# Kernel tuning notes

Hardware: AMD Instinct MI355X
Metric: run time of the kernel (lower is better)

The kernel has to match this reference:

```python
import jax, jax.numpy as jnp
import numpy as np

IN_FEATURES = 4096
OUT_FEATURES = 14336
TOPK_RATIO = 0.3
TOPK = int(IN_FEATURES * TOPK_RATIO)  # 1228


def setup_inputs() -> dict:
    key = jax.random.key(0)
    k1, k2, k3 = jax.random.split(key, 3)
    x = jax.random.normal(k1, (1, 1, IN_FEATURES), dtype=jnp.float32)
    weight = jax.random.normal(k2, (OUT_FEATURES, IN_FEATURES), dtype=jnp.float32)
    bias = jax.random.normal(k3, (OUT_FEATURES,), dtype=jnp.float32)
    return {"x": x, "weight": weight, "bias": bias}


def reference(x, weight, bias):
    # Decode path (bsz*seq == 1), first-call cache miss: indices come from
    # the current activation's top-k |x| values (recall==1.0 branch).
    bsz, seq, _ = x.shape
    xf = x.reshape(-1)  # [in_features]
    # argsort(|x|, descending)[:topk] == top_k on |x| (tie order irrelevant for the math)
    _, idx = jax.lax.top_k(jnp.abs(xf).astype(jnp.float32), TOPK)  # [topk]
    x_slice = xf[idx]                 # [topk]
    w_slice = weight[:, idx]          # [out_features, topk]
    # x[:, indices] @ weight_slice.T + bias
    out = jnp.einsum("k,ok->o", x_slice, w_slice) + bias  # [out_features]
    return out.reshape(bsz, seq, OUT_FEATURES)
```

## Files before the change

### kernel.cpp

```cpp
#include <hip/hip_runtime.h>
#include <hip/hip_bf16.h>

#define N_IN 4096
#define N_OUT 14336
#define TOPK 1228

__global__ __launch_bounds__(1024) void topk_mask_kernel(
    const float* __restrict__ x, float* __restrict__ x_masked) {
  __shared__ unsigned int s_abs[N_IN];
  __shared__ unsigned int s_hist[256];
  __shared__ unsigned int s_scan[256];
  __shared__ unsigned int s_prefix;
  __shared__ unsigned int s_krem;
  __shared__ unsigned long long s_cmask[N_IN / 64];
  __shared__ unsigned int s_cbase[N_IN / 64];

  const int tid = threadIdx.x;
  const int lane = tid & 63;

#pragma unroll
  for (int it = 0; it < N_IN / 1024; ++it) {
    const int i = it * 1024 + tid;
    s_abs[i] = __float_as_uint(x[i]) & 0x7fffffffu;
  }
  if (tid == 0) { s_prefix = 0u; s_krem = TOPK; }
  __syncthreads();

  for (int pass = 3; pass >= 0; --pass) {
    if (tid < 256) s_hist[tid] = 0u;
    __syncthreads();
    const int shift = pass * 8;
    const unsigned int maskAbove =
        (pass == 3) ? 0u : (0xFFFFFFFFu << (shift + 8));
    const unsigned int prefix = s_prefix;
    const unsigned int krem = s_krem;

#pragma unroll
    for (int it = 0; it < N_IN / 1024; ++it) {
      const int i = it * 1024 + tid;
      const unsigned int b = s_abs[i];
      const bool active = ((b & maskAbove) == prefix);
      const unsigned int bucket = (b >> shift) & 0xFFu;
      unsigned long long m = __ballot(active);
#pragma unroll
      for (int bit = 0; bit < 8; ++bit) {
        const unsigned long long vote =
            __ballot(active && ((bucket >> bit) & 1u));
        m &= ((bucket >> bit) & 1u) ? vote : ~vote;
      }
      if (active) {
        const int leader = __ffsll((unsigned long long)m) - 1;
        if (lane == leader)
          atomicAdd(&s_hist[bucket], (unsigned int)__popcll(m));
      }
    }
    __syncthreads();

    if (tid < 256) s_scan[tid] = s_hist[255 - tid];
    __syncthreads();
    for (int off = 1; off < 256; off <<= 1) {
      unsigned int v = 0u;
      if (tid < 256 && tid >= off) v = s_scan[tid - off];
      __syncthreads();
      if (tid < 256) s_scan[tid] += v;
      __syncthreads();
    }
    if (tid < 256) {
      const unsigned int t = (unsigned int)tid;
      const unsigned int C = s_scan[255 - t];
      const unsigned int S = (t == 255u) ? 0u : s_scan[254 - t];
      if (S < krem && C >= krem) {
        s_prefix = prefix | (t << shift);
        s_krem = krem - S;
      }
    }
    __syncthreads();
  }

  const unsigned int t_abs = s_prefix;
  const unsigned int need = s_krem;

#pragma unroll
  for (int it = 0; it < N_IN / 1024; ++it) {
    const int i = it * 1024 + tid;
    const bool eq = (s_abs[i] == t_abs);
    const unsigned long long m = __ballot(eq);
    if (lane == 0) s_cmask[i >> 6] = m;
  }
  __syncthreads();
  if (tid < 64) {
    const unsigned int cnt = (unsigned int)__popcll(s_cmask[tid]);
    unsigned int inc = cnt;
#pragma unroll
    for (int off = 1; off < 64; off <<= 1) {
      const unsigned int v = __shfl_up(inc, off, 64);
      if (lane >= off) inc += v;
    }
    s_cbase[tid] = inc - cnt;
  }
  __syncthreads();

#pragma unroll
  for (int it = 0; it < N_IN / 1024; ++it) {
    const int i = it * 1024 + tid;
    const unsigned int b = s_abs[i];
    bool sel = (b > t_abs);
    if (b == t_abs) {
      const unsigned long long below =
          s_cmask[i >> 6] & ((1ull << lane) - 1ull);
      sel = (s_cbase[i >> 6] + (unsigned int)__popcll(below)) < need;
    }
    x_masked[i] = sel ? x[i] : 0.0f;
  }
}

__global__ __launch_bounds__(256) void masked_matvec_kernel(
    const float* __restrict__ xm, const float* __restrict__ W,
    const float* __restrict__ bias, float* __restrict__ out) {
  __shared__ float s_x[N_IN];

  const int tid = threadIdx.x;
  for (int i = tid; i < N_IN; i += 256) s_x[i] = xm[i];
  __syncthreads();

  const int wave = tid >> 6;
  const int lane = tid & 63;
  const int row = blockIdx.x * 4 + wave;
  const float* wr = W + (size_t)row * N_IN;

  float acc = 0.0f;
#pragma unroll
  for (int it = 0; it < N_IN / 256; ++it) {
    const int base = it * 256 + lane * 4;
    const float4 w = *reinterpret_cast<const float4*>(wr + base);
    const float4 xv = *reinterpret_cast<const float4*>(&s_x[base]);
    acc += w.x * xv.x + w.y * xv.y + w.z * xv.z + w.w * xv.w;
  }

#pragma unroll
  for (int off = 32; off >= 1; off >>= 1) acc += __shfl_down(acc, off, 64);

  if (lane == 0) out[row] = acc + bias[row];
}

extern "C" void kernel_launch(void* const* d_in, const int* in_sizes, int n_in,
                              void* d_out, int out_size, void* d_ws,
                              size_t ws_size, hipStream_t stream) {
  const float* x    = (const float*)d_in[0];
  const float* W    = (const float*)d_in[1];
  const float* bias = (const float*)d_in[2];
  float* out = (float*)d_out;
  float* xm  = (float*)d_ws;

  topk_mask_kernel<<<1, 1024, 0, stream>>>(x, xm);
  masked_matvec_kernel<<<N_OUT / 4, 256, 0, stream>>>(xm, W, bias, out);
}
```

Before: 58.13 us.

## Fuse top-k selection into matvec blocks and prefetch weight rows early

Merges the single-block top-k mask kernel and the matvec kernel into one launch. Each of the 3584 blocks now recomputes the radix select on its own shared copy of x. The first weight loads are issued before the selection so they overlap it. The 256-bin scan is replaced by a wave-level shuffle scan, and a fast path skips tie handling when all threshold-equal elements are needed. This removes the serialized single-block kernel and the extra launch, but every block repeats the selection work, which could lengthen per-block latency on a kernel that is bandwidth-bound.

```diff
diff --git a/kernel.cpp b/kernel.cpp
--- a/kernel.cpp
+++ b/kernel.cpp
@@ -4,43 +4,58 @@
 #define N_IN 4096
 #define N_OUT 14336
 #define TOPK 1228
+#define PF 4
 
-__global__ __launch_bounds__(1024) void topk_mask_kernel(
-    const float* __restrict__ x, float* __restrict__ x_masked) {
-  __shared__ unsigned int s_abs[N_IN];
-  __shared__ unsigned int s_hist[256];
-  __shared__ unsigned int s_scan[256];
-  __shared__ unsigned int s_prefix;
-  __shared__ unsigned int s_krem;
+__global__ __launch_bounds__(256) void fused_topk_matvec_kernel(
+    const float* __restrict__ x, const float* __restrict__ W,
+    const float* __restrict__ bias, float* __restrict__ out) {
+  __shared__ __align__(16) float s_x[N_IN];
+  __shared__ __align__(16) unsigned int s_hist[256];
+  __shared__ unsigned int s_pk[4];
   __shared__ unsigned long long s_cmask[N_IN / 64];
   __shared__ unsigned int s_cbase[N_IN / 64];
 
   const int tid = threadIdx.x;
+  const int wave = tid >> 6;
   const int lane = tid & 63;
+  const int row = blockIdx.x * 4 + wave;
 
-#pragma unroll
-  for (int it = 0; it < N_IN / 1024; ++it) {
-    const int i = it * 1024 + tid;
-    s_abs[i] = __float_as_uint(x[i]) & 0x7fffffffu;
-  }
-  if (tid == 0) { s_prefix = 0u; s_krem = TOPK; }
+  const float4* __restrict__ x4 = reinterpret_cast<const float4*>(x);
+  const float4* __restrict__ wr4 =
+      reinterpret_cast<const float4*>(W + (size_t)row * N_IN);
+  float4* s_x4 = reinterpret_cast<float4*>(s_x);
+
+  float4 xv0 = x4[0 * 256 + tid];
+  float4 xv1 = x4[1 * 256 + tid];
+  float4 xv2 = x4[2 * 256 + tid];
+  float4 xv3 = x4[3 * 256 + tid];
+  float4 w0 = wr4[0 * 64 + lane];
+  float4 w1 = wr4[1 * 64 + lane];
+  float4 w2 = wr4[2 * 64 + lane];
+  float4 w3 = wr4[3 * 64 + lane];
+
+  s_x4[0 * 256 + tid] = xv0;
+  s_x4[1 * 256 + tid] = xv1;
+  s_x4[2 * 256 + tid] = xv2;
+  s_x4[3 * 256 + tid] = xv3;
+  if (tid == 0) { s_pk[0] = 0u; s_pk[1] = TOPK; }
   __syncthreads();
 
   for (int pass = 3; pass >= 0; --pass) {
-    if (tid < 256) s_hist[tid] = 0u;
+    const unsigned int prefix = s_pk[0];
+    const unsigned int krem = s_pk[1];
+    s_hist[tid] = 0u;
     __syncthreads();
+
     const int shift = pass * 8;
     const unsigned int maskAbove =
         (pass == 3) ? 0u : (0xFFFFFFFFu << (shift + 8));
-    const unsigned int prefix = s_prefix;
-    const unsigned int krem = s_krem;
 
-#pragma unroll
-    for (int it = 0; it < N_IN / 1024; ++it) {
-      const int i = it * 1024 + tid;
-      const unsigned int b = s_abs[i];
-      const bool active = ((b & maskAbove) == prefix);
-      const unsigned int bucket = (b >> shift) & 0xFFu;
+    for (int r = 0; r < 16; ++r) {
+      const unsigned int ub =
+          __float_as_uint(s_x[r * 256 + tid]) & 0x7fffffffu;
+      const bool active = ((ub & maskAbove) == prefix);
+      const unsigned int bucket = (ub >> shift) & 0xFFu;
       unsigned long long m = __ballot(active);
 #pragma unroll
       for (int bit = 0; bit < 8; ++bit) {
@@ -56,84 +71,95 @@
     }
     __syncthreads();
 
-    if (tid < 256) s_scan[tid] = s_hist[255 - tid];
-    __syncthreads();
-    for (int off = 1; off < 256; off <<= 1) {
-      unsigned int v = 0u;
-      if (tid < 256 && tid >= off) v = s_scan[tid - off];
-      __syncthreads();
-      if (tid < 256) s_scan[tid] += v;
-      __syncthreads();
-    }
-    if (tid < 256) {
-      const unsigned int t = (unsigned int)tid;
-      const unsigned int C = s_scan[255 - t];
-      const unsigned int S = (t == 255u) ? 0u : s_scan[254 - t];
-      if (S < krem && C >= krem) {
-        s_prefix = prefix | (t << shift);
-        s_krem = krem - S;
+    if (tid < 64) {
+      const unsigned int h0 = s_hist[tid * 4 + 0];
+      const unsigned int h1 = s_hist[tid * 4 + 1];
+      const unsigned int h2 = s_hist[tid * 4 + 2];
+      const unsigned int h3 = s_hist[tid * 4 + 3];
+      const unsigned int s = h0 + h1 + h2 + h3;
+      unsigned int inc = s;
+#pragma unroll
+      for (int off = 1; off < 64; off <<= 1) {
+        const unsigned int v = __shfl_down(inc, off, 64);
+        if (tid + off < 64) inc += v;
+      }
+      const unsigned int U = inc - s;
+      const unsigned int C3 = U + h3;
+      const unsigned int C2 = C3 + h2;
+      const unsigned int C1 = C2 + h1;
+      const unsigned int C0 = C1 + h0;
+      const unsigned int Carr[4] = {C0, C1, C2, C3};
+      const unsigned int Sarr[4] = {C1, C2, C3, U};
+      const unsigned int hv[4] = {h0, h1, h2, h3};
+#pragma unroll
+      for (int j = 0; j < 4; ++j) {
+        if (Sarr[j] < krem && krem <= Carr[j]) {
+          s_pk[0] = prefix | ((unsigned int)(tid * 4 + j) << shift);
+          s_pk[1] = krem - Sarr[j];
+          s_pk[2] = hv[j];
+        }
       }
     }
     __syncthreads();
   }
 
-  const unsigned int t_abs = s_prefix;
-  const unsigned int need = s_krem;
+  const unsigned int t_abs = s_pk[0];
+  const unsigned int need = s_pk[1];
+  const unsigned int eqc = s_pk[2];
 
+  if (eqc == need) {
+    for (int r = 0; r < 16; ++r) {
+      const int i = r * 256 + tid;
+      if ((__float_as_uint(s_x[i]) & 0x7fffffffu) < t_abs) s_x[i] = 0.0f;
+    }
+  } else {
+    for (int r = 0; r < 16; ++r) {
+      const int i = r * 256 + tid;
+      const bool eq = ((__float_as_uint(s_x[i]) & 0x7fffffffu) == t_abs);
+      const unsigned long long m = __ballot(eq);
+      if (lane == 0) s_cmask[r * 4 + wave] = m;
+    }
+    __syncthreads();
+    if (tid < 64) {
+      const unsigned int cnt = (unsigned int)__popcll(s_cmask[tid]);
+      unsigned int inc = cnt;
 #pragma unroll
-  for (int it = 0; it < N_IN / 1024; ++it) {
-    const int i = it * 1024 + tid;
-    const bool eq = (s_abs[i] == t_abs);
-    const unsigned long long m = __ballot(eq);
-    if (lane == 0) s_cmask[i >> 6] = m;
-  }
-  __syncthreads();
-  if (tid < 64) {
-    const unsigned int cnt = (unsigned int)__popcll(s_cmask[tid]);
-    unsigned int inc = cnt;
-#pragma unroll
-    for (int off = 1; off < 64; off <<= 1) {
-      const unsigned int v = __shfl_up(inc, off, 64);
-      if (lane >= off) inc += v;
+      for (int off = 1; off < 64; off <<= 1) {
+        const unsigned int v = __shfl_up(inc, off, 64);
+        if (tid >= off) inc += v;
+      }
+      s_cbase[tid] = inc - cnt;
     }
-    s_cbase[tid] = inc - cnt;
+    __syncthreads();
+    for (int r = 0; r < 16; ++r) {
+      const int i = r * 256 + tid;
+      const unsigned int ub = __float_as_uint(s_x[i]) & 0x7fffffffu;
+      bool sel = (ub > t_abs);
+      if (ub == t_abs) {
+        const unsigned long long below =
+            s_cmask[r * 4 + wave] & ((1ull << lane) - 1ull);
+        sel = (s_cbase[r * 4 + wave] + (unsigned int)__popcll(below)) < need;
+      }
+      if (!sel) s_x[i] = 0.0f;
+    }
   }
   __syncthreads();
 
+  float acc = 0.0f;
+  {
+    const float4 v0 = s_x4[0 * 64 + lane];
+    acc += w0.x * v0.x + w0.y * v0.y + w0.z * v0.z + w0.w * v0.w;
+    const float4 v1 = s_x4[1 * 64 + lane];
+    acc += w1.x * v1.x + w1.y * v1.y + w1.z * v1.z + w1.w * v1.w;
+    const float4 v2 = s_x4[2 * 64 + lane];
+    acc += w2.x * v2.x + w2.y * v2.y + w2.z * v2.z + w2.w * v2.w;
+    const float4 v3 = s_x4[3 * 64 + lane];
+    acc += w3.x * v3.x + w3.y * v3.y + w3.z * v3.z + w3.w * v3.w;
+  }
 #pragma unroll
-  for (int it = 0; it < N_IN / 1024; ++it) {
-    const int i = it * 1024 + tid;
-    const unsigned int b = s_abs[i];
-    bool sel = (b > t_abs);
-    if (b == t_abs) {
-      const unsigned long long below =
-          s_cmask[i >> 6] & ((1ull << lane) - 1ull);
-      sel = (s_cbase[i >> 6] + (unsigned int)__popcll(below)) < need;
-    }
-    x_masked[i] = sel ? x[i] : 0.0f;
-  }
-}
-
-__global__ __launch_bounds__(256) void masked_matvec_kernel(
-    const float* __restrict__ xm, const float* __restrict__ W,
-    const float* __restrict__ bias, float* __restrict__ out) {
-  __shared__ float s_x[N_IN];
-
-  const int tid = threadIdx.x;
-  for (int i = tid; i < N_IN; i += 256) s_x[i] = xm[i];
-  __syncthreads();
-
-  const int wave = tid >> 6;
-  const int lane = tid & 63;
-  const int row = blockIdx.x * 4 + wave;
-  const float* wr = W + (size_t)row * N_IN;
-
-  float acc = 0.0f;
-#pragma unroll
-  for (int it = 0; it < N_IN / 256; ++it) {
-    const int base = it * 256 + lane * 4;
-    const float4 w = *reinterpret_cast<const float4*>(wr + base);
-    const float4 xv = *reinterpret_cast<const float4*>(&s_x[base]);
+  for (int it = PF; it < N_IN / 256; ++it) {
+    const float4 w = wr4[it * 64 + lane];
+    const float4 xv = s_x4[it * 64 + lane];
     acc += w.x * xv.x + w.y * xv.y + w.z * xv.z + w.w * xv.w;
   }
 
@@ -150,8 +176,6 @@
   const float* W    = (const float*)d_in[1];
   const float* bias = (const float*)d_in[2];
   float* out = (float*)d_out;
-  float* xm  = (float*)d_ws;
 
-  topk_mask_kernel<<<1, 1024, 0, stream>>>(x, xm);
-  masked_matvec_kernel<<<N_OUT / 4, 256, 0, stream>>>(xm, W, bias, out);
+  fused_topk_matvec_kernel<<<N_OUT / 4, 256, 0, stream>>>(x, W, bias, out);
 }
```

Result: slower. 102.6 us (+76.4%).
